# Kernel tuning notes

Hardware: AMD Instinct MI355X
Metric: run time of the kernel (lower is better)

## Reference

```python
import jax, jax.numpy as jnp
import numpy as np

D_MODEL = 2048
N_HEADS = 16
HEAD_DIM = D_MODEL // N_HEADS  # 128
HIDDEN = int(8 * D_MODEL / 3)  # 5461
EPS = 1e-6


def setup_inputs() -> dict:
    key = jax.random.key(0)
    ks = jax.random.split(key, 12)
    B, S = 2, 2048
    std = D_MODEL ** -0.5
    return {
        "x": jax.random.normal(ks[0], (B, S, D_MODEL), jnp.float32),
        "freq_cis": jax.random.normal(ks[1], (S, HEAD_DIM // 2, 2, 2), jnp.float32),
        "wq": jax.random.normal(ks[2], (D_MODEL, D_MODEL), jnp.float32) * std,
        "wk": jax.random.normal(ks[3], (D_MODEL, D_MODEL), jnp.float32) * std,
        "wv": jax.random.normal(ks[4], (D_MODEL, D_MODEL), jnp.float32) * std,
        "wo": jax.random.normal(ks[5], (D_MODEL, D_MODEL), jnp.float32) * std,
        "bo": jnp.zeros((D_MODEL,), jnp.float32),
        "w1": jax.random.normal(ks[6], (HIDDEN, D_MODEL), jnp.float32) * std,
        "w3": jax.random.normal(ks[7], (HIDDEN, D_MODEL), jnp.float32) * std,
        "w2": jax.random.normal(ks[8], (D_MODEL, HIDDEN), jnp.float32) * (HIDDEN ** -0.5),
        "g_attn": jnp.ones((D_MODEL,), jnp.float32),
        "g_ffn": jnp.ones((D_MODEL,), jnp.float32),
    }


def rmsnorm(x, g):
    xf = x.astype(jnp.float32)
    return xf * jax.lax.rsqrt(jnp.mean(xf * xf, axis=-1, keepdims=True) + EPS) * g


def rope(xq, xk, f):
    # xq/xk: [b, s, h, hd]; f: [s, hd/2, 2, 2]
    b, s, h, hd = xq.shape
    xq_ = xq.reshape(b, s, h, hd // 2, 2)
    xk_ = xk.reshape(b, s, h, hd // 2, 2)
    # out[b,s,h,i,j] = sum_k x[b,s,h,i,k] * f[s,i,j,k]
    q = jnp.einsum("bshik,sijk->bshij", xq_, f).reshape(b, s, h, hd)
    k = jnp.einsum("bshik,sijk->bshij", xk_, f).reshape(b, s, h, hd)
    return q, k


def reference(x, freq_cis, wq, wk, wv, wo, bo, w1, w3, w2, g_attn, g_ffn):
    b, s, d = x.shape
    h, hd = N_HEADS, HEAD_DIM
    scale = hd ** -0.5

    # --- attention sublayer ---
    xn = rmsnorm(x, g_attn)
    q = jnp.einsum("bsd,ed->bse", xn, wq).reshape(b, s, h, hd)
    k = jnp.einsum("bsd,ed->bse", xn, wk).reshape(b, s, h, hd)
    v = jnp.einsum("bsd,ed->bse", xn, wv).reshape(b, s, h, hd)
    q, k = rope(q, k, freq_cis[:s])
    attn = jnp.einsum("bqhd,bkhd->bhqk", q, k) * scale
    attn = jax.nn.softmax(attn, axis=-1)
    o = jnp.einsum("bhqk,bkhd->bqhd", attn, v).reshape(b, s, d)
    o = jnp.einsum("bsd,ed->bse", o, wo) + bo
    hres = x + o

    # --- SwiGLU FFN sublayer ---
    hn = rmsnorm(hres, g_ffn)
    x1 = jnp.einsum("bsd,hd->bsh", hn, w1)
    x3 = jnp.einsum("bsd,hd->bsh", hn, w3)
    ffn = jnp.einsum("bsh,dh->bsd", jax.nn.silu(x1) * x3, w2)
    return hres + ffn
```

## Files before the change

kernel.cpp:

```cpp
#include <hip/hip_runtime.h>

#define D_MODEL 2048
#define NHEADS 16
#define HDIM 128
#define HIDDEN_ 5461
#define HP2 5632
#define BATCH 2
#define SEQ 2048
#define MTOK 4096

typedef unsigned short u16;
typedef __attribute__((ext_vector_type(8))) short bf16x8;
typedef __attribute__((ext_vector_type(4))) float f32x4;
typedef __attribute__((ext_vector_type(4))) short s16x4;

__device__ __forceinline__ u16 f2b(float f) {
  union { float f; unsigned u; } v; v.f = f;
  return (u16)((v.u + 0x7FFFu + ((v.u >> 16) & 1u)) >> 16);
}
__device__ __forceinline__ float b2f(u16 u) {
  union { unsigned u; float f; } v; v.u = ((unsigned)u) << 16;
  return v.f;
}
__device__ __forceinline__ void gload16(const void* g, void* l) {
  __builtin_amdgcn_global_load_lds(
      (const __attribute__((address_space(1))) unsigned int*)g,
      (__attribute__((address_space(3))) unsigned int*)l, 16, 0, 0);
}

#define SB0() __builtin_amdgcn_sched_barrier(0)
#define BARRIER() do { SB0(); __builtin_amdgcn_s_barrier(); SB0(); } while (0)
#define LGKM0() do { asm volatile("s_waitcnt lgkmcnt(0)" ::: "memory"); SB0(); } while (0)

__global__ __launch_bounds__(256) void k_conv8(const float* __restrict__ src,
                                               u16* __restrict__ dst, int n8) {
  int stride = gridDim.x * 256;
  for (int i = blockIdx.x * 256 + threadIdx.x; i < n8; i += stride) {
    const float4* s = (const float4*)src + (size_t)i * 2;
    float4 a = s[0], b = s[1];
    bf16x8 o;
    o[0] = f2b(a.x); o[1] = f2b(a.y); o[2] = f2b(a.z); o[3] = f2b(a.w);
    o[4] = f2b(b.x); o[5] = f2b(b.y); o[6] = f2b(b.z); o[7] = f2b(b.w);
    ((bf16x8*)dst)[i] = o;
  }
}

__global__ __launch_bounds__(256) void k_conv3(const float* __restrict__ s0,
                                               const float* __restrict__ s1,
                                               const float* __restrict__ s2,
                                               u16* __restrict__ dst) {
  const int n8 = D_MODEL * D_MODEL / 8;
  int total = 3 * n8;
  int stride = gridDim.x * 256;
  for (int i = blockIdx.x * 256 + threadIdx.x; i < total; i += stride) {
    int seg = i >> 19, j = i & (n8 - 1);
    const float* s = (seg == 0) ? s0 : (seg == 1 ? s1 : s2);
    const float4* sp = (const float4*)s + (size_t)j * 2;
    float4 a = sp[0], b = sp[1];
    bf16x8 o;
    o[0] = f2b(a.x); o[1] = f2b(a.y); o[2] = f2b(a.z); o[3] = f2b(a.w);
    o[4] = f2b(b.x); o[5] = f2b(b.y); o[6] = f2b(b.z); o[7] = f2b(b.w);
    ((bf16x8*)dst)[i] = o;
  }
}

__global__ __launch_bounds__(256) void k_convrows(const float* __restrict__ src,
                                                  u16* __restrict__ dst,
                                                  int n8src, int n8dst) {
  int stride = gridDim.x * 256;
  for (int i = blockIdx.x * 256 + threadIdx.x; i < n8dst; i += stride) {
    bf16x8 o;
    if (i < n8src) {
      const float4* sp = (const float4*)src + (size_t)i * 2;
      float4 a = sp[0], b = sp[1];
      o[0] = f2b(a.x); o[1] = f2b(a.y); o[2] = f2b(a.z); o[3] = f2b(a.w);
      o[4] = f2b(b.x); o[5] = f2b(b.y); o[6] = f2b(b.z); o[7] = f2b(b.w);
    } else {
      o = (bf16x8){0, 0, 0, 0, 0, 0, 0, 0};
    }
    ((bf16x8*)dst)[i] = o;
  }
}

__global__ __launch_bounds__(256) void k_convpad(const float* __restrict__ src,
                                                 u16* __restrict__ dst,
                                                 int srows, int scols, int drows, int dcols) {
  size_t n = (size_t)drows * dcols;
  size_t stride = (size_t)gridDim.x * 256;
  for (size_t i = blockIdx.x * 256 + threadIdx.x; i < n; i += stride) {
    int r = (int)(i / dcols), c = (int)(i % dcols);
    float v = (r < srows && c < scols) ? src[(size_t)r * scols + c] : 0.f;
    dst[i] = f2b(v);
  }
}

__global__ __launch_bounds__(256) void k_silumul(u16* __restrict__ X1,
                                                 const u16* __restrict__ X3, int n8) {
  int stride = gridDim.x * 256;
  for (int i = blockIdx.x * 256 + threadIdx.x; i < n8; i += stride) {
    bf16x8 a = ((const bf16x8*)X1)[i];
    bf16x8 b = ((const bf16x8*)X3)[i];
    bf16x8 o;
#pragma unroll
    for (int e = 0; e < 8; e++) {
      float v1 = b2f((u16)a[e]);
      float v3 = b2f((u16)b[e]);
      float sig = 1.f / (1.f + __expf(-v1));
      o[e] = f2b(v1 * sig * v3);
    }
    ((bf16x8*)X1)[i] = o;
  }
}

__global__ __launch_bounds__(256) void k_rmsnorm(const float* __restrict__ X,
                                                 const float* __restrict__ G,
                                                 u16* __restrict__ Out) {
  int row = blockIdx.x;
  int tid = threadIdx.x;
  const float4* x4 = (const float4*)(X + (size_t)row * D_MODEL);
  float4 a = x4[tid * 2], b = x4[tid * 2 + 1];
  float ss = a.x * a.x + a.y * a.y + a.z * a.z + a.w * a.w +
             b.x * b.x + b.y * b.y + b.z * b.z + b.w * b.w;
#pragma unroll
  for (int off = 1; off < 64; off <<= 1) ss += __shfl_xor(ss, off);
  __shared__ float part[4];
  if ((tid & 63) == 0) part[tid >> 6] = ss;
  __syncthreads();
  float rstd = rsqrtf((part[0] + part[1] + part[2] + part[3]) * (1.0f / D_MODEL) + 1e-6f);
  const float4* g4 = (const float4*)G;
  float4 ga = g4[tid * 2], gb = g4[tid * 2 + 1];
  bf16x8 o;
  o[0] = f2b(a.x * rstd * ga.x); o[1] = f2b(a.y * rstd * ga.y);
  o[2] = f2b(a.z * rstd * ga.z); o[3] = f2b(a.w * rstd * ga.w);
  o[4] = f2b(b.x * rstd * gb.x); o[5] = f2b(b.y * rstd * gb.y);
  o[6] = f2b(b.z * rstd * gb.z); o[7] = f2b(b.w * rstd * gb.w);
  *((bf16x8*)(Out + (size_t)row * D_MODEL) + tid) = o;
}

template <int WN, int EPI>
__global__ __launch_bounds__(512, 2) void k_gemm2(const u16* __restrict__ A,
                                                  const u16* __restrict__ Bw,
                                                  const u16* __restrict__ Bw2,
                                                  void* __restrict__ O0,
                                                  void* __restrict__ O1,
                                                  void* __restrict__ O2,
                                                  const float* __restrict__ bias,
                                                  const float* __restrict__ res,
                                                  const u16* __restrict__ aux,
                                                  int M, int N, int K) {
  constexpr int BN = WN * 64;
  constexpr int PB = BN * 64;
  __shared__ __align__(128) char lds[65536 + 4 * PB];
  const int tid = threadIdx.x;
  const int w = tid >> 6, lane = tid & 63;
  const int lo = lane & 15, hi = lane >> 4;
  const int wr = w >> 2, wc = w & 3;

  const int ntN = N / BN;
  const int nwg = gridDim.x * gridDim.y;
  const int flat = blockIdx.y * gridDim.x + blockIdx.x;
  const int swz = (flat & 7) * (nwg >> 3) + (flat >> 3);
  const int tm = swz / ntN, tn = swz % ntN;
  const int m0 = tm * 256, n0 = tn * BN;

  const u16* bbase;
  if (EPI == 5)
    bbase = (n0 < 5632) ? Bw + (size_t)n0 * K : Bw2 + (size_t)(n0 - 5632) * K;
  else
    bbase = Bw + (size_t)n0 * K;

  auto stA = [&](int nb, int kk, int k0) {
#pragma unroll
    for (int j = 0; j < 2; ++j) {
      int row = j * 128 + (tid >> 2);
      const u16* g = A + (size_t)(m0 + row) * K + k0 + kk * 32 + (tid & 3) * 8;
      gload16(g, lds + nb * 32768 + kk * 16384 + j * 8192 + tid * 16);
    }
  };
  auto stB = [&](int nb, int kk, int k0) {
#pragma unroll
    for (int j = 0; j < WN / 2; ++j) {
      int row = j * 128 + (tid >> 2);
      const u16* g = bbase + (size_t)row * K + k0 + kk * 32 + (tid & 3) * 8;
      gload16(g, lds + 65536 + nb * 2 * PB + kk * PB + j * 8192 + tid * 16);
    }
  };
  auto ldA = [&](int buf, int kk, int mf) {
    return *(const bf16x8*)(lds + buf * 32768 + kk * 16384 +
                            (wr * 128 + mf * 16 + lo) * 64 + hi * 16);
  };
  auto ldB = [&](int buf, int kk, int nf) {
    return *(const bf16x8*)(lds + 65536 + buf * 2 * PB + kk * PB +
                            (wc * (WN * 16) + nf * 16 + lo) * 64 + hi * 16);
  };
#define VMCNT_CONFIRM()                                             \
  do {                                                              \
    if constexpr (WN == 4)                                          \
      asm volatile("s_waitcnt vmcnt(4)" ::: "memory");              \
    else                                                            \
      asm volatile("s_waitcnt vmcnt(3)" ::: "memory");              \
    SB0();                                                          \
  } while (0)

  f32x4 acc[8][WN];
#pragma unroll
  for (int i = 0; i < 8; i++)
#pragma unroll
    for (int j = 0; j < WN; j++) acc[i][j] = (f32x4){0.f, 0.f, 0.f, 0.f};

  stA(0, 0, 0);
  stB(0, 0, 0);
  stA(0, 1, 0);
  stB(0, 1, 0);
  VMCNT_CONFIRM();
  BARRIER();

  const int KT = K / 64;
  for (int kt = 0; kt < KT; ++kt) {
    const int buf = kt & 1, nb = buf ^ 1;
    int kn = (kt + 1) * 64;
    if (kn >= K) kn = 0;
    bf16x8 aF[4], bF[WN];

#pragma unroll
    for (int i = 0; i < 4; i++) aF[i] = ldA(buf, 0, i);
#pragma unroll
    for (int j = 0; j < WN; j++) bF[j] = ldB(buf, 0, j);
    stA(nb, 0, kn);
    BARRIER();
    LGKM0();
    __builtin_amdgcn_s_setprio(1);
#pragma unroll
    for (int i = 0; i < 4; i++)
#pragma unroll
      for (int j = 0; j < WN; j++)
        acc[i][j] = __builtin_amdgcn_mfma_f32_16x16x32_bf16(aF[i], bF[j], acc[i][j], 0, 0, 0);
    __builtin_amdgcn_s_setprio(0);
    BARRIER();

#pragma unroll
    for (int i = 0; i < 4; i++) aF[i] = ldA(buf, 0, 4 + i);
    stB(nb, 0, kn);
    VMCNT_CONFIRM();
    BARRIER();
    LGKM0();
    __builtin_amdgcn_s_setprio(1);
#pragma unroll
    for (int i = 0; i < 4; i++)
#pragma unroll
      for (int j = 0; j < WN; j++)
        acc[4 + i][j] = __builtin_amdgcn_mfma_f32_16x16x32_bf16(aF[i], bF[j], acc[4 + i][j], 0, 0, 0);
    __builtin_amdgcn_s_setprio(0);
    BARRIER();

#pragma unroll
    for (int i = 0; i < 4; i++) aF[i] = ldA(buf, 1, i);
#pragma unroll
    for (int j = 0; j < WN; j++) bF[j] = ldB(buf, 1, j);
    stA(nb, 1, kn);
    BARRIER();
    LGKM0();
    __builtin_amdgcn_s_setprio(1);
#pragma unroll
    for (int i = 0; i < 4; i++)
#pragma unroll
      for (int j = 0; j < WN; j++)
        acc[i][j] = __builtin_amdgcn_mfma_f32_16x16x32_bf16(aF[i], bF[j], acc[i][j], 0, 0, 0);
    __builtin_amdgcn_s_setprio(0);
    BARRIER();

#pragma unroll
    for (int i = 0; i < 4; i++) aF[i] = ldA(buf, 1, 4 + i);
    stB(nb, 1, kn);
    VMCNT_CONFIRM();
    BARRIER();
    LGKM0();
    __builtin_amdgcn_s_setprio(1);
#pragma unroll
    for (int i = 0; i < 4; i++)
#pragma unroll
      for (int j = 0; j < WN; j++)
        acc[4 + i][j] = __builtin_amdgcn_mfma_f32_16x16x32_bf16(aF[i], bF[j], acc[4 + i][j], 0, 0, 0);
    __builtin_amdgcn_s_setprio(0);
    BARRIER();
  }

  u16* qkvout = nullptr;
  int c0 = 0;
  if (EPI == 1) {
    int seg = n0 >> 11;
    qkvout = (u16*)(seg == 0 ? O0 : (seg == 1 ? O1 : O2));
    c0 = n0 & 2047;
  }
  u16* w13out = nullptr;
  int w13c0 = 0;
  if (EPI == 5) {
    w13out = (u16*)(n0 < 5632 ? O0 : O1);
    w13c0 = (n0 < 5632) ? n0 : n0 - 5632;
  }
#pragma unroll
  for (int i = 0; i < 8; i++) {
#pragma unroll
    for (int j = 0; j < WN; j++) {
      int colL = wc * (WN * 16) + j * 16 + lo;
#pragma unroll
      for (int r = 0; r < 4; r++) {
        int row = m0 + wr * 128 + i * 16 + hi * 4 + r;
        float v = acc[i][j][r];
        if (EPI == 0) {
          ((u16*)O0)[(size_t)row * N + n0 + colL] = f2b(v);
        } else if (EPI == 1) {
          qkvout[(size_t)row * 2048 + c0 + colL] = f2b(v);
        } else if (EPI == 2) {
          size_t idx = (size_t)row * N + n0 + colL;
          ((float*)O0)[idx] = v + bias[n0 + colL] + res[idx];
        } else if (EPI == 3) {
          size_t idx = (size_t)row * N + n0 + colL;
          ((float*)O0)[idx] = v + res[idx];
        } else if (EPI == 4) {
          size_t idx = (size_t)row * N + n0 + colL;
          float v1 = b2f(aux[idx]);
          float sig = 1.f / (1.f + __expf(-v1));
          ((u16*)O0)[idx] = f2b(v1 * sig * v);
        } else {
          w13out[(size_t)row * 5632 + w13c0 + colL] = f2b(v);
        }
      }
    }
  }
#undef VMCNT_CONFIRM
}

__global__ __launch_bounds__(256) void k_rope(u16* __restrict__ Qb, u16* __restrict__ Kb,
                                              const float* __restrict__ F) {
  int n = MTOK * (D_MODEL / 2);
  int stride = gridDim.x * 256;
  for (int t = blockIdx.x * 256 + threadIdx.x; t < n; t += stride) {
    int i = t & 63;
    int rest = t >> 6;
    int hh = rest & 15;
    int tok = rest >> 4;
    int s = tok & (SEQ - 1);
    float4 f = ((const float4*)F)[s * 64 + i];
    size_t off = (size_t)tok * D_MODEL + hh * HDIM + i * 2;
    float x0 = b2f(Qb[off]), x1 = b2f(Qb[off + 1]);
    Qb[off] = f2b(x0 * f.x + x1 * f.y);
    Qb[off + 1] = f2b(x0 * f.z + x1 * f.w);
    x0 = b2f(Kb[off]); x1 = b2f(Kb[off + 1]);
    Kb[off] = f2b(x0 * f.x + x1 * f.y);
    Kb[off + 1] = f2b(x0 * f.z + x1 * f.w);
  }
}

__global__ __launch_bounds__(256) void k_vt(const u16* __restrict__ V, u16* __restrict__ VT) {
  __shared__ u16 t[64][72];
  const int stile = blockIdx.x;
  const int bh = blockIdx.y;
  const int dz = blockIdx.z;
  const int b = bh >> 4, h = bh & 15;
  const int tok0 = b * SEQ + stile * 64;
  const int d0 = dz * 64;
  const int tid = threadIdx.x;
#pragma unroll
  for (int p = 0; p < 2; p++) {
    int idx = p * 256 + tid;
    int row = idx >> 3, seg = idx & 7;
    bf16x8 v = *(const bf16x8*)(V + (size_t)(tok0 + row) * D_MODEL + h * HDIM + d0 + seg * 8);
    *(bf16x8*)(&t[row][seg * 8]) = v;
  }
  __syncthreads();
#pragma unroll
  for (int p = 0; p < 2; p++) {
    int idx = p * 256 + tid;
    int dr = idx >> 3, seg = idx & 7;
    bf16x8 o;
#pragma unroll
    for (int e = 0; e < 8; e++) o[e] = t[seg * 8 + e][dr];
    *(bf16x8*)(VT + ((size_t)bh * HDIM + d0 + dr) * SEQ + stile * 64 + seg * 8) = o;
  }
}

__global__ __launch_bounds__(256) void k_flash4(const u16* __restrict__ Q,
                                                const u16* __restrict__ Kb,
                                                const u16* __restrict__ VT,
                                                u16* __restrict__ O) {
  __shared__ u16 Kt[64 * 128];
  __shared__ u16 Vt[128 * 64];
  __shared__ u16 Pl[4][2][16 * 72];
  const int tid = threadIdx.x;
  const int w = tid >> 6, lane = tid & 63;
  const int lo = lane & 15, hi = lane >> 4;
  const int qt = blockIdx.x, bh = blockIdx.y;
  const int b = bh >> 4, h = bh & 15;
  const size_t qrow0 = (size_t)b * SEQ + qt * 128 + w * 32;
  const float SC = 0.08838834764831845f * 1.4426950408889634f;

  bf16x8 aQ[2][4];
#pragma unroll
  for (int qg = 0; qg < 2; qg++)
#pragma unroll
    for (int kb = 0; kb < 4; kb++)
      aQ[qg][kb] = *(const bf16x8*)(Q + (qrow0 + qg * 16 + lo) * D_MODEL + h * HDIM + kb * 32 + hi * 8);

  float m_s[2] = {-3.0e38f, -3.0e38f}, l_s[2] = {0.f, 0.f};
  f32x4 oacc[2][8];
#pragma unroll
  for (int qg = 0; qg < 2; qg++)
#pragma unroll
    for (int d = 0; d < 8; d++) oacc[qg][d] = (f32x4){0.f, 0.f, 0.f, 0.f};

  const int krowL = tid >> 4;
  const int kslot = (tid & 15) ^ (krowL & 7);
  const int vrowL = tid >> 3;
  const int vslot = (tid & 7) ^ (vrowL & 7);
  const u16* Kbase = Kb + (size_t)b * SEQ * D_MODEL + h * HDIM;
  const u16* Vbase = VT + (size_t)bh * HDIM * SEQ;
  unsigned* Plw = (unsigned*)&Pl[w][0][0];

  bf16x8 kreg[4], vreg[4];
  auto issue = [&](int kt) {
#pragma unroll
    for (int t = 0; t < 4; t++) {
      int row = t * 16 + krowL;
      kreg[t] = *(const bf16x8*)(Kbase + (size_t)(kt * 64 + row) * D_MODEL + kslot * 8);
    }
#pragma unroll
    for (int t = 0; t < 4; t++) {
      int row = t * 32 + vrowL;
      vreg[t] = *(const bf16x8*)(Vbase + (size_t)row * SEQ + kt * 64 + vslot * 8);
    }
  };
  auto commit = [&]() {
#pragma unroll
    for (int t = 0; t < 4; t++)
      *(bf16x8*)((char*)Kt + t * 4096 + tid * 16) = kreg[t];
#pragma unroll
    for (int t = 0; t < 4; t++)
      *(bf16x8*)((char*)Vt + t * 4096 + tid * 16) = vreg[t];
  };

  issue(0);
  commit();
  BARRIER();

  const int NT = SEQ / 64;
  for (int kt = 0; kt < NT; kt++) {
    if (kt + 1 < NT) {
      issue(kt + 1);
      SB0();
    }

    f32x4 sf[2][4];
#pragma unroll
    for (int cb = 0; cb < 4; cb++) {
      bf16x8 kA[4];
#pragma unroll
      for (int kb = 0; kb < 4; kb++) {
        int ps = (kb * 4 + hi) ^ (lo & 7);
        kA[kb] = *(const bf16x8*)(Kt + (cb * 16 + lo) * 128 + ps * 8);
      }
#pragma unroll
      for (int qg = 0; qg < 2; qg++) {
        f32x4 s = (f32x4){0.f, 0.f, 0.f, 0.f};
#pragma unroll
        for (int kb = 0; kb < 4; kb++)
          s = __builtin_amdgcn_mfma_f32_16x16x32_bf16(kA[kb], aQ[qg][kb], s, 0, 0, 0);
        sf[qg][cb] = s;
      }
    }

    float tsc[2];
    bool ok = true;
#pragma unroll
    for (int qg = 0; qg < 2; qg++) {
      float t0 = fmaxf(fmaxf(sf[qg][0][0], sf[qg][0][1]), fmaxf(sf[qg][0][2], sf[qg][0][3]));
      float t1 = fmaxf(fmaxf(sf[qg][1][0], sf[qg][1][1]), fmaxf(sf[qg][1][2], sf[qg][1][3]));
      float t2 = fmaxf(fmaxf(sf[qg][2][0], sf[qg][2][1]), fmaxf(sf[qg][2][2], sf[qg][2][3]));
      float t3 = fmaxf(fmaxf(sf[qg][3][0], sf[qg][3][1]), fmaxf(sf[qg][3][2], sf[qg][3][3]));
      float t = fmaxf(fmaxf(t0, t1), fmaxf(t2, t3));
      t = fmaxf(t, __shfl_xor(t, 16));
      t = fmaxf(t, __shfl_xor(t, 32));
      tsc[qg] = t * SC;
      ok = ok && (tsc[qg] - m_s[qg] <= 11.5f);
    }
    bool skip = __all(ok);
#pragma unroll
    for (int qg = 0; qg < 2; qg++) {
      float mm = m_s[qg];
      if (!skip) {
        mm = fmaxf(m_s[qg], tsc[qg]);
        float alpha = exp2f(m_s[qg] - mm);
        l_s[qg] *= alpha;
#pragma unroll
        for (int d = 0; d < 8; d++) oacc[qg][d] *= alpha;
        m_s[qg] = mm;
      }
      float rs = 0.f;
#pragma unroll
      for (int cb = 0; cb < 4; cb++) {
        float p0 = exp2f(sf[qg][cb][0] * SC - mm);
        float p1 = exp2f(sf[qg][cb][1] * SC - mm);
        float p2 = exp2f(sf[qg][cb][2] * SC - mm);
        float p3 = exp2f(sf[qg][cb][3] * SC - mm);
        rs += (p0 + p1) + (p2 + p3);
        unsigned pk0, pk1;
        asm("v_cvt_pk_bf16_f32 %0, %1, %2" : "=v"(pk0) : "v"(p0), "v"(p1));
        asm("v_cvt_pk_bf16_f32 %0, %1, %2" : "=v"(pk1) : "v"(p2), "v"(p3));
        Plw[qg * 576 + lo * 36 + cb * 8 + hi * 2 + 0] = pk0;
        Plw[qg * 576 + lo * 36 + cb * 8 + hi * 2 + 1] = pk1;
      }
      rs += __shfl_xor(rs, 16);
      rs += __shfl_xor(rs, 32);
      l_s[qg] += rs;
    }
    LGKM0();

    bf16x8 aP[2][2];
#pragma unroll
    for (int qg = 0; qg < 2; qg++)
#pragma unroll
      for (int ks = 0; ks < 2; ks++)
        aP[qg][ks] = *(const bf16x8*)(&Pl[w][qg][lo * 72 + ks * 32 + hi * 8]);
#pragma unroll
    for (int db = 0; db < 8; db++) {
      bf16x8 vA[2];
#pragma unroll
      for (int ks = 0; ks < 2; ks++) {
        int ps = (ks * 4 + hi) ^ (lo & 7);
        vA[ks] = *(const bf16x8*)(Vt + (db * 16 + lo) * 64 + ps * 8);
      }
#pragma unroll
      for (int qg = 0; qg < 2; qg++)
#pragma unroll
        for (int ks = 0; ks < 2; ks++)
          oacc[qg][db] = __builtin_amdgcn_mfma_f32_16x16x32_bf16(vA[ks], aP[qg][ks], oacc[qg][db], 0, 0, 0);
    }

    if (kt + 1 < NT) {
      BARRIER();
      commit();
      BARRIER();
    }
  }

#pragma unroll
  for (int qg = 0; qg < 2; qg++) {
    float inv = 1.f / l_s[qg];
    size_t rowoff = (qrow0 + qg * 16 + lo) * D_MODEL + h * HDIM;
#pragma unroll
    for (int db = 0; db < 8; db++) {
      s16x4 o;
#pragma unroll
      for (int r = 0; r < 4; r++) o[r] = (short)f2b(oacc[qg][db][r] * inv);
      *(s16x4*)(O + rowoff + db * 16 + hi * 4) = o;
    }
  }
}

extern "C" void kernel_launch(void* const* d_in, const int* in_sizes, int n_in,
                              void* d_out, int out_size, void* d_ws, size_t ws_size,
                              hipStream_t stream) {
  (void)in_sizes; (void)n_in; (void)out_size; (void)ws_size;
  const float* x  = (const float*)d_in[0];
  const float* fc = (const float*)d_in[1];
  const float* wq = (const float*)d_in[2];
  const float* wk = (const float*)d_in[3];
  const float* wv = (const float*)d_in[4];
  const float* wo = (const float*)d_in[5];
  const float* bo = (const float*)d_in[6];
  const float* w1 = (const float*)d_in[7];
  const float* w3 = (const float*)d_in[8];
  const float* w2 = (const float*)d_in[9];
  const float* ga = (const float*)d_in[10];
  const float* gf = (const float*)d_in[11];
  float* out = (float*)d_out;

  char* p = (char*)d_ws;
  auto alloc = [&](size_t bytes) { char* r = p; p += (bytes + 255) & ~(size_t)255; return r; };
  u16* xn  = (u16*)alloc((size_t)MTOK * D_MODEL * 2);
  u16* qb  = (u16*)alloc((size_t)MTOK * D_MODEL * 2);
  u16* kb  = (u16*)alloc((size_t)MTOK * D_MODEL * 2);
  u16* vb  = (u16*)alloc((size_t)MTOK * D_MODEL * 2);
  u16* x1  = (u16*)alloc((size_t)MTOK * HP2 * 2);
  u16* x3  = (u16*)alloc((size_t)MTOK * HP2 * 2);
  u16* wsl = (u16*)alloc((size_t)3 * D_MODEL * D_MODEL * 2);
  u16* vbt = xn;
  u16* ob  = vb;
  u16* hn  = qb;
  u16* w3b = kb;

  k_rmsnorm<<<MTOK, 256, 0, stream>>>(x, ga, xn);
  k_conv3<<<1536, 256, 0, stream>>>(wq, wk, wv, wsl);
  k_gemm2<4, 1><<<dim3(6144 / 256, MTOK / 256), 512, 0, stream>>>(
      xn, wsl, nullptr, qb, kb, vb, nullptr, nullptr, nullptr, MTOK, 6144, D_MODEL);
  k_rope<<<1024, 256, 0, stream>>>(qb, kb, fc);
  k_vt<<<dim3(SEQ / 64, BATCH * NHEADS, 2), 256, 0, stream>>>(vb, vbt);
  dim3 gfl(SEQ / 128, BATCH * NHEADS);
  k_flash4<<<gfl, 256, 0, stream>>>(qb, kb, vbt, ob);
  k_conv8<<<1024, 256, 0, stream>>>(wo, wsl, D_MODEL * D_MODEL / 8);
  k_gemm2<2, 2><<<dim3(2048 / 128, MTOK / 256), 512, 0, stream>>>(
      ob, wsl, nullptr, out, nullptr, nullptr, bo, x, nullptr, MTOK, D_MODEL, D_MODEL);

  k_rmsnorm<<<MTOK, 256, 0, stream>>>(out, gf, hn);
  k_convrows<<<1024, 256, 0, stream>>>(w1, wsl, HIDDEN_ * D_MODEL / 8, HP2 * D_MODEL / 8);
  k_convrows<<<1024, 256, 0, stream>>>(w3, w3b, HIDDEN_ * D_MODEL / 8, HP2 * D_MODEL / 8);
  k_gemm2<4, 5><<<dim3(11264 / 256, MTOK / 256), 512, 0, stream>>>(
      hn, wsl, w3b, x1, x3, nullptr, nullptr, nullptr, nullptr, MTOK, 11264, D_MODEL);
  k_silumul<<<2048, 256, 0, stream>>>(x1, x3, MTOK * HP2 / 8);
  k_convpad<<<1024, 256, 0, stream>>>(w2, wsl, D_MODEL, HIDDEN_, D_MODEL, HP2);
  k_gemm2<2, 3><<<dim3(2048 / 128, MTOK / 256), 512, 0, stream>>>(
      x1, wsl, nullptr, out, nullptr, nullptr, nullptr, out, nullptr, MTOK, D_MODEL, HP2);
}
```

Baseline: 739.2 us.

## Interleave w1/w3 rows and fuse SiLU-multiply into the W13 GEMM epilogue

The W1 and W3 weights are converted into one bf16 buffer in which blocks of 128 w1 rows and 128 w3 rows alternate, so each 256-column GEMM tile holds matching x1 and x3 columns. The new epilogue stages the x3 half in LDS, then combines it with the x1 accumulators to apply silu(x1)*x3 and writes only the gated result. This removes the separate SiLU-multiply kernel and the write and re-read of the x3 intermediate, and merges two conversion launches into one. In exchange it needs a barrier, LDS traffic in the epilogue, and only half the waves do the final stores.

```diff
diff --git a/kernel.cpp b/kernel.cpp
--- a/kernel.cpp
+++ b/kernel.cpp
@@ -64,14 +64,19 @@
   }
 }
 
-__global__ __launch_bounds__(256) void k_convrows(const float* __restrict__ src,
-                                                  u16* __restrict__ dst,
-                                                  int n8src, int n8dst) {
+__global__ __launch_bounds__(256) void k_convw13(const float* __restrict__ w1,
+                                                 const float* __restrict__ w3,
+                                                 u16* __restrict__ dst) {
+  const int n8 = (11264 * D_MODEL) / 8;
   int stride = gridDim.x * 256;
-  for (int i = blockIdx.x * 256 + threadIdx.x; i < n8dst; i += stride) {
+  for (int i = blockIdx.x * 256 + threadIdx.x; i < n8; i += stride) {
+    int r = i >> 8, c8 = i & 255;
+    int t = r & 255;
+    int srow = ((r >> 8) << 7) + (t & 127);
     bf16x8 o;
-    if (i < n8src) {
-      const float4* sp = (const float4*)src + (size_t)i * 2;
+    if (srow < HIDDEN_) {
+      const float* s = (t < 128) ? w1 : w3;
+      const float4* sp = (const float4*)(s + (size_t)srow * D_MODEL + c8 * 8);
       float4 a = sp[0], b = sp[1];
       o[0] = f2b(a.x); o[1] = f2b(a.y); o[2] = f2b(a.z); o[3] = f2b(a.w);
       o[4] = f2b(b.x); o[5] = f2b(b.y); o[6] = f2b(b.z); o[7] = f2b(b.w);
@@ -91,24 +96,6 @@
     int r = (int)(i / dcols), c = (int)(i % dcols);
     float v = (r < srows && c < scols) ? src[(size_t)r * scols + c] : 0.f;
     dst[i] = f2b(v);
-  }
-}
-
-__global__ __launch_bounds__(256) void k_silumul(u16* __restrict__ X1,
-                                                 const u16* __restrict__ X3, int n8) {
-  int stride = gridDim.x * 256;
-  for (int i = blockIdx.x * 256 + threadIdx.x; i < n8; i += stride) {
-    bf16x8 a = ((const bf16x8*)X1)[i];
-    bf16x8 b = ((const bf16x8*)X3)[i];
-    bf16x8 o;
-#pragma unroll
-    for (int e = 0; e < 8; e++) {
-      float v1 = b2f((u16)a[e]);
-      float v3 = b2f((u16)b[e]);
-      float sig = 1.f / (1.f + __expf(-v1));
-      o[e] = f2b(v1 * sig * v3);
-    }
-    ((bf16x8*)X1)[i] = o;
   }
 }
 
@@ -285,6 +272,41 @@
     BARRIER();
   }
 
+  if (EPI == 6) {
+    u16* xls = (u16*)lds;
+    if (wc >= 2) {
+#pragma unroll
+      for (int i = 0; i < 8; i++)
+#pragma unroll
+        for (int j = 0; j < WN; j++) {
+          int col = (wc - 2) * 64 + j * 16 + lo;
+#pragma unroll
+          for (int r = 0; r < 4; r++) {
+            int row = wr * 128 + i * 16 + hi * 4 + r;
+            xls[row * 132 + col] = f2b(acc[i][j][r]);
+          }
+        }
+    }
+    BARRIER();
+    if (wc < 2) {
+      int c0 = n0 >> 1;
+#pragma unroll
+      for (int i = 0; i < 8; i++)
+#pragma unroll
+        for (int j = 0; j < WN; j++) {
+          int colL = wc * 64 + j * 16 + lo;
+#pragma unroll
+          for (int r = 0; r < 4; r++) {
+            int rowL = wr * 128 + i * 16 + hi * 4 + r;
+            float v1 = acc[i][j][r];
+            float v3 = b2f(xls[rowL * 132 + colL]);
+            float sig = 1.f / (1.f + __expf(-v1));
+            ((u16*)O0)[(size_t)(m0 + rowL) * 5632 + c0 + colL] = f2b(v1 * sig * v3);
+          }
+        }
+    }
+    return;
+  }
   u16* qkvout = nullptr;
   int c0 = 0;
   if (EPI == 1) {
@@ -317,12 +339,7 @@
         } else if (EPI == 3) {
           size_t idx = (size_t)row * N + n0 + colL;
           ((float*)O0)[idx] = v + res[idx];
-        } else if (EPI == 4) {
-          size_t idx = (size_t)row * N + n0 + colL;
-          float v1 = b2f(aux[idx]);
-          float sig = 1.f / (1.f + __expf(-v1));
-          ((u16*)O0)[idx] = f2b(v1 * sig * v);
-        } else {
+        } else if (EPI == 5) {
           w13out[(size_t)row * 5632 + w13c0 + colL] = f2b(v);
         }
       }
@@ -577,17 +594,16 @@
 
   char* p = (char*)d_ws;
   auto alloc = [&](size_t bytes) { char* r = p; p += (bytes + 255) & ~(size_t)255; return r; };
-  u16* xn  = (u16*)alloc((size_t)MTOK * D_MODEL * 2);
-  u16* qb  = (u16*)alloc((size_t)MTOK * D_MODEL * 2);
-  u16* kb  = (u16*)alloc((size_t)MTOK * D_MODEL * 2);
-  u16* vb  = (u16*)alloc((size_t)MTOK * D_MODEL * 2);
-  u16* x1  = (u16*)alloc((size_t)MTOK * HP2 * 2);
-  u16* x3  = (u16*)alloc((size_t)MTOK * HP2 * 2);
-  u16* wsl = (u16*)alloc((size_t)3 * D_MODEL * D_MODEL * 2);
+  u16* xn   = (u16*)alloc((size_t)MTOK * D_MODEL * 2);
+  u16* qb   = (u16*)alloc((size_t)MTOK * D_MODEL * 2);
+  u16* kb   = (u16*)alloc((size_t)MTOK * D_MODEL * 2);
+  u16* vb   = (u16*)alloc((size_t)MTOK * D_MODEL * 2);
+  u16* x1   = (u16*)alloc((size_t)MTOK * HP2 * 2);
+  u16* w13i = (u16*)alloc((size_t)11264 * D_MODEL * 2);
+  u16* wsl  = (u16*)alloc((size_t)3 * D_MODEL * D_MODEL * 2);
   u16* vbt = xn;
   u16* ob  = vb;
   u16* hn  = qb;
-  u16* w3b = kb;
 
   k_rmsnorm<<<MTOK, 256, 0, stream>>>(x, ga, xn);
   k_conv3<<<1536, 256, 0, stream>>>(wq, wk, wv, wsl);
@@ -602,11 +618,9 @@
       ob, wsl, nullptr, out, nullptr, nullptr, bo, x, nullptr, MTOK, D_MODEL, D_MODEL);
 
   k_rmsnorm<<<MTOK, 256, 0, stream>>>(out, gf, hn);
-  k_convrows<<<1024, 256, 0, stream>>>(w1, wsl, HIDDEN_ * D_MODEL / 8, HP2 * D_MODEL / 8);
-  k_convrows<<<1024, 256, 0, stream>>>(w3, w3b, HIDDEN_ * D_MODEL / 8, HP2 * D_MODEL / 8);
-  k_gemm2<4, 5><<<dim3(11264 / 256, MTOK / 256), 512, 0, stream>>>(
-      hn, wsl, w3b, x1, x3, nullptr, nullptr, nullptr, nullptr, MTOK, 11264, D_MODEL);
-  k_silumul<<<2048, 256, 0, stream>>>(x1, x3, MTOK * HP2 / 8);
+  k_convw13<<<2048, 256, 0, stream>>>(w1, w3, w13i);
+  k_gemm2<4, 6><<<dim3(11264 / 256, MTOK / 256), 512, 0, stream>>>(
+      hn, w13i, nullptr, x1, nullptr, nullptr, nullptr, nullptr, nullptr, MTOK, 11264, D_MODEL);
   k_convpad<<<1024, 256, 0, stream>>>(w2, wsl, D_MODEL, HIDDEN_, D_MODEL, HP2);
   k_gemm2<2, 3><<<dim3(2048 / 128, MTOK / 256), 512, 0, stream>>>(
       x1, wsl, nullptr, out, nullptr, nullptr, nullptr, out, nullptr, MTOK, D_MODEL, HP2);
```

After: 734.0 us. No clear change (-0.7%).
